# Optimization experiments

Hardware: AMD Instinct MI355X
Metric: run time of the kernel (lower is better)

## Reference

```python
import jax, jax.numpy as jnp
import numpy as np
from jax import lax

FILTER_SIZE = 3
C_IN = 128
C_OUT = 256
PAD = 1
STRIDE = 1


def setup_inputs() -> dict:
    key = jax.random.key(0)
    k1, k2 = jax.random.split(key)
    prev_a = jax.random.normal(k1, (32, 56, 56, C_IN), dtype=jnp.float32)
    # filter_w initialized ~ N(0, 1) as in the original tf.random.normal
    filter_w = jax.random.normal(k2, (FILTER_SIZE, FILTER_SIZE, C_IN, C_OUT), dtype=jnp.float32)
    filter_b = jnp.zeros((1, 1, 1, C_OUT), dtype=jnp.float32)
    return {"prev_a": prev_a, "filter_w": filter_w, "filter_b": filter_b}


def reference(prev_a, filter_w, filter_b):
    # NHWC input, HWIO filter -> NHWC output; same math as the nested-loop conv:
    # z[i,h,w,c] = sum(prev_a_pad[i, h*s:h*s+f, w*s:w*s+f, :] * W[:,:,:,c]) + b[c]
    z = lax.conv_general_dilated(
        prev_a,
        filter_w,
        window_strides=(STRIDE, STRIDE),
        padding=[(PAD, PAD), (PAD, PAD)],
        dimension_numbers=("NHWC", "HWIO", "NHWC"),
    )
    z = z + filter_b  # bias broadcast over (m, H, W)
    return jax.nn.relu(z)
```

## Files before the change

kernel.cpp:

```cpp
#include <hip/hip_runtime.h>
#include <hip/hip_bf16.h>


#define NIMG 32
#define HH 56
#define WW 56
#define PH 58
#define PW 58
#define CIN 128
#define COUT 256
#define KTOT 1152
#define PAD_ELEMS (NIMG * PH * PW * CIN)

#define BK 64
#define NT (KTOT / BK)
#define NBLK ((NIMG * HH * WW) / 256)

typedef __attribute__((ext_vector_type(8))) short bf16x8;
typedef __attribute__((ext_vector_type(4))) short s16x4;
typedef __attribute__((ext_vector_type(4))) float f32x4;

__device__ __forceinline__ short f2bf(float x) {
    union { __hip_bfloat16 b; short s; } u;
    u.b = __float2bfloat16(x);
    return u.s;
}

typedef const void __attribute__((address_space(1)))* gas1_t;
typedef void __attribute__((address_space(3)))* las3_t;
__device__ __forceinline__ void async16(short* lds_p, const short* g) {
    __builtin_amdgcn_global_load_lds((gas1_t)g, (las3_t)lds_p, 16, 0, 0);
}

__global__ __launch_bounds__(256) void pack_input(const float* __restrict__ in,
                                                  short* __restrict__ pad) {
    const int tid  = blockIdx.x * 256 + threadIdx.x;
    const int flat = tid * 8;
    const int c8   = flat & (CIN - 1);
    const int rest = flat >> 7;
    const int iw   = rest % PW;
    const int r2   = rest / PW;
    const int ih   = r2 % PH;
    const int img  = r2 / PH;
    bf16x8 v = (bf16x8)0;
    if (ih >= 1 && ih <= HH && iw >= 1 && iw <= WW) {
        const float* p = in + (((size_t)(img * HH + ih - 1) * WW + (iw - 1)) * CIN + c8);
        const float4 x0 = *(const float4*)p;
        const float4 x1 = *(const float4*)(p + 4);
        v.s0 = f2bf(x0.x); v.s1 = f2bf(x0.y); v.s2 = f2bf(x0.z); v.s3 = f2bf(x0.w);
        v.s4 = f2bf(x1.x); v.s5 = f2bf(x1.y); v.s6 = f2bf(x1.z); v.s7 = f2bf(x1.w);
    }
    *(bf16x8*)(pad + flat) = v;
}

__global__ __launch_bounds__(256) void pack_wgt(const float* __restrict__ w,
                                                short* __restrict__ wt) {
    __shared__ short tile[32][33];
    const int k0 = blockIdx.x * 32;
    const int n0 = blockIdx.y * 32;
    const int t  = threadIdx.x;
    {
        const int kl  = t >> 3;
        const int nl4 = (t & 7) * 4;
        const float4 x = *(const float4*)(w + (size_t)(k0 + kl) * COUT + n0 + nl4);
        tile[kl][nl4 + 0] = f2bf(x.x);
        tile[kl][nl4 + 1] = f2bf(x.y);
        tile[kl][nl4 + 2] = f2bf(x.z);
        tile[kl][nl4 + 3] = f2bf(x.w);
    }
    __syncthreads();
    {
        const int nl  = t >> 3;
        const int kl4 = (t & 7) * 4;
        s16x4 v;
        v.x = tile[kl4 + 0][nl];
        v.y = tile[kl4 + 1][nl];
        v.z = tile[kl4 + 2][nl];
        v.w = tile[kl4 + 3][nl];
        *(s16x4*)(wt + (size_t)(n0 + nl) * KTOT + k0 + kl4) = v;
    }
}

#define FENCE() asm volatile("" ::: "memory")
#define BARRIER() do { FENCE(); __builtin_amdgcn_s_barrier(); FENCE(); } while (0)
#define VMWAIT(N) asm volatile("s_waitcnt vmcnt(" #N ")" ::: "memory")
#define NOSTMT ((void)0)

__global__ __launch_bounds__(512, 2) void conv_mfma(const short* __restrict__ apad,
                                                    const short* __restrict__ bwt,
                                                    const float* __restrict__ bias,
                                                    float* __restrict__ out) {
    __shared__ short lds[65536];

    const int t  = threadIdx.x;
    const int l  = t & 63;
    const int w  = t >> 6;
    const int wm = w >> 2;
    const int wn = w & 3;
    const int fr = l & 15;
    const int fq = l >> 4;

    const int laneoff = fr * 32 + ((fq ^ ((fr >> 1) & 3))) * 8;
    const int kcs   = (t & 3) ^ ((t >> 3) & 3);
    const int wbase = w * 512;

    const int bid = blockIdx.x;
    const int swz = (bid & 7) * (NBLK / 8) + (bid >> 3);
    const int m0  = swz * 256;

    const int r0 = t >> 2;
    int abase0, abase1;
    {
        int m = m0 + r0;
        int img = m / (HH * WW), rem = m - img * (HH * WW);
        int oh = rem / WW, ow = rem - oh * WW;
        abase0 = ((img * PH + oh) * PW + ow) * CIN;
        m = m0 + r0 + 128;
        img = m / (HH * WW); rem = m - img * (HH * WW);
        oh = rem / WW; ow = rem - oh * WW;
        abase1 = ((img * PH + oh) * PW + ow) * CIN;
    }
    const int bbase0 = r0 * KTOT;
    const int bbase1 = (r0 + 128) * KTOT;

    f32x4 acc[8][4];
#pragma unroll
    for (int i = 0; i < 8; ++i)
#pragma unroll
        for (int j = 0; j < 4; ++j) { f32x4 z = {0.f, 0.f, 0.f, 0.f}; acc[i][j] = z; }

    bf16x8 af[8];

#define STAGE_A(KT, KH) do {                                                  \
        const int _tap = (KT) >> 1;                                           \
        const int _fh  = (_tap * 11) >> 5;                   \
        const int _fw  = _tap - 3 * _fh;                                      \
        const int _off = (_fh * PW + _fw) * CIN + ((KT) & 1) * 64             \
                         + (KH) * 32 + kcs * 8;                               \
        short* _l = lds + (((KT) & 1) * 2 + (KH)) * 8192 + wbase;             \
        async16(_l,        apad + abase0 + _off);                             \
        async16(_l + 4096, apad + abase1 + _off);                             \
    } while (0)

#define STAGE_B(KT, KH) do {                                                  \
        const int _off = (KT) * 64 + (KH) * 32 + kcs * 8;                     \
        short* _l = lds + 32768 + (((KT) & 1) * 2 + (KH)) * 8192 + wbase;     \
        async16(_l,        bwt + bbase0 + _off);                              \
        async16(_l + 4096, bwt + bbase1 + _off);                              \
    } while (0)

#define PHASE(BUF, KH, NH, STAGE_STMT, WAIT_STMT) do {                        \
        const short* _a = lds + ((BUF) * 2 + (KH)) * 8192;                    \
        const short* _b = lds + 32768 + ((BUF) * 2 + (KH)) * 8192;            \
        bf16x8 _bf0, _bf1;                                                    \
        if ((NH) == 0) {                                                      \
            _Pragma("unroll")                                                 \
            for (int _i = 0; _i < 8; ++_i)                                    \
                af[_i] = *(const bf16x8*)(_a + wm * 4096 + _i * 512 + laneoff); \
        }                                                                     \
        _bf0 = *(const bf16x8*)(_b + wn * 2048 + (NH) * 1024 +   0 + laneoff); \
        _bf1 = *(const bf16x8*)(_b + wn * 2048 + (NH) * 1024 + 512 + laneoff); \
        STAGE_STMT;                                                           \
        BARRIER();                                                            \
        __builtin_amdgcn_s_setprio(1);                                        \
        _Pragma("unroll")                                                     \
        for (int _i = 0; _i < 8; ++_i) {                                      \
            acc[_i][(NH)*2+0] = __builtin_amdgcn_mfma_f32_16x16x32_bf16(      \
                af[_i], _bf0, acc[_i][(NH)*2+0], 0, 0, 0);                    \
            acc[_i][(NH)*2+1] = __builtin_amdgcn_mfma_f32_16x16x32_bf16(      \
                af[_i], _bf1, acc[_i][(NH)*2+1], 0, 0, 0);                    \
        }                                                                     \
        __builtin_amdgcn_s_setprio(0);                                        \
        WAIT_STMT;                                                            \
        BARRIER();                                                            \
    } while (0)

    STAGE_A(0, 0); STAGE_B(0, 0);
    STAGE_A(0, 1); STAGE_B(0, 1);
    STAGE_A(1, 0); STAGE_B(1, 0);
    VMWAIT(8);
    BARRIER();

#pragma unroll 1
    for (int kt = 0; kt < NT - 2; kt += 2) {
        PHASE(0, 0, 0, STAGE_A(kt + 1, 1), NOSTMT);
        PHASE(0, 0, 1, STAGE_B(kt + 1, 1), VMWAIT(8));
        PHASE(0, 1, 0, STAGE_A(kt + 2, 0), NOSTMT);
        PHASE(0, 1, 1, STAGE_B(kt + 2, 0), VMWAIT(8));
        PHASE(1, 0, 0, STAGE_A(kt + 2, 1), NOSTMT);
        PHASE(1, 0, 1, STAGE_B(kt + 2, 1), VMWAIT(8));
        PHASE(1, 1, 0, STAGE_A(kt + 3, 0), NOSTMT);
        PHASE(1, 1, 1, STAGE_B(kt + 3, 0), VMWAIT(8));
    }
    PHASE(0, 0, 0, STAGE_A(NT - 1, 1), NOSTMT);
    PHASE(0, 0, 1, STAGE_B(NT - 1, 1), VMWAIT(8));
    PHASE(0, 1, 0, NOSTMT,             NOSTMT);
    PHASE(0, 1, 1, NOSTMT,             VMWAIT(4));
    PHASE(1, 0, 0, NOSTMT,             NOSTMT);
    PHASE(1, 0, 1, NOSTMT,             VMWAIT(0));
    PHASE(1, 1, 0, NOSTMT,             NOSTMT);
    PHASE(1, 1, 1, NOSTMT,             NOSTMT);

#pragma unroll
    for (int j = 0; j < 4; ++j) {
        const int n  = wn * 64 + j * 16 + fr;
        const float bj = bias[n];
#pragma unroll
        for (int i = 0; i < 8; ++i) {
            const int mr = m0 + wm * 128 + i * 16 + fq * 4;
#pragma unroll
            for (int r = 0; r < 4; ++r) {
                const float v = acc[i][j][r] + bj;
                out[(size_t)(mr + r) * COUT + n] = v > 0.f ? v : 0.f;
            }
        }
    }
#undef STAGE_A
#undef STAGE_B
#undef PHASE
}

extern "C" void kernel_launch(void* const* d_in, const int* in_sizes, int n_in,
                              void* d_out, int out_size, void* d_ws, size_t ws_size,
                              hipStream_t stream) {
    const float* in   = (const float*)d_in[0];
    const float* wgt  = (const float*)d_in[1];
    const float* bias = (const float*)d_in[2];
    float* out = (float*)d_out;

    short* pad = (short*)d_ws;
    short* wt  = (short*)d_ws + PAD_ELEMS;

    pack_input<<<PAD_ELEMS / 8 / 256, 256, 0, stream>>>(in, pad);
    pack_wgt<<<dim3(KTOT / 32, COUT / 32), 256, 0, stream>>>(wgt, wt);

    conv_mfma<<<NBLK, 512, 0, stream>>>(pad, wt, bias, out);
}
```

Before: 205.0 us.

## Shrink conv M-tile to 224 rows and restructure MFMA phases

Changes the block M-tile from 256 to 224 output pixels, so there are 448 blocks instead of 392 and each block does less work. The 2-blocks-per-CU slots on the device are used more evenly and the critical path per block gets shorter. The LDS layout, A staging and accumulator tiling are reworked to 7x4 fragments per wave. Each k-step now splits into one phase with 4 A rows and 4 B columns and a second phase with the remaining 3 A rows. Waves 6 and 7 issue redundant duplicate A loads into already-written slots. The lower ratio of MFMA work to loads per block may reduce efficiency.

```diff
diff --git a/kernel.cpp b/kernel.cpp
--- a/kernel.cpp
+++ b/kernel.cpp
@@ -12,9 +12,14 @@
 #define KTOT 1152
 #define PAD_ELEMS (NIMG * PH * PW * CIN)
 
+#define BM 224
 #define BK 64
 #define NT (KTOT / BK)
-#define NBLK ((NIMG * HH * WW) / 256)
+#define NBLK ((NIMG * HH * WW) / BM)
+
+#define AREG_SZ 7168
+#define BREG_BASE 28672
+#define BREG_SZ 8192
 
 typedef __attribute__((ext_vector_type(8))) short bf16x8;
 typedef __attribute__((ext_vector_type(4))) short s16x4;
@@ -90,7 +95,7 @@
                                                     const short* __restrict__ bwt,
                                                     const float* __restrict__ bias,
                                                     float* __restrict__ out) {
-    __shared__ short lds[65536];
+    __shared__ short lds[61440];
 
     const int t  = threadIdx.x;
     const int l  = t & 63;
@@ -101,12 +106,13 @@
     const int fq = l >> 4;
 
     const int laneoff = fr * 32 + ((fq ^ ((fr >> 1) & 3))) * 8;
-    const int kcs   = (t & 3) ^ ((t >> 3) & 3);
-    const int wbase = w * 512;
+    const int afb = wm * 3584;
+    const int bfb = wn * 2048;
+    const int kcs = (t & 3) ^ ((t >> 3) & 3);
 
     const int bid = blockIdx.x;
     const int swz = (bid & 7) * (NBLK / 8) + (bid >> 3);
-    const int m0  = swz * 256;
+    const int m0  = swz * BM;
 
     const int r0 = t >> 2;
     int abase0, abase1;
@@ -115,21 +121,26 @@
         int img = m / (HH * WW), rem = m - img * (HH * WW);
         int oh = rem / WW, ow = rem - oh * WW;
         abase0 = ((img * PH + oh) * PW + ow) * CIN;
-        m = m0 + r0 + 128;
-        img = m / (HH * WW); rem = m - img * (HH * WW);
-        oh = rem / WW; ow = rem - oh * WW;
-        abase1 = ((img * PH + oh) * PW + ow) * CIN;
-    }
+        if (t < 384) {
+            m = m0 + r0 + 128;
+            img = m / (HH * WW); rem = m - img * (HH * WW);
+            oh = rem / WW; ow = rem - oh * WW;
+            abase1 = ((img * PH + oh) * PW + ow) * CIN;
+        } else {
+            abase1 = abase0;
+        }
+    }
+    const int a2lds = (w < 6) ? (4096 + w * 512) : (w * 512);
     const int bbase0 = r0 * KTOT;
     const int bbase1 = (r0 + 128) * KTOT;
 
-    f32x4 acc[8][4];
-#pragma unroll
-    for (int i = 0; i < 8; ++i)
+    f32x4 acc[7][4];
+#pragma unroll
+    for (int i = 0; i < 7; ++i)
 #pragma unroll
         for (int j = 0; j < 4; ++j) { f32x4 z = {0.f, 0.f, 0.f, 0.f}; acc[i][j] = z; }
 
-    bf16x8 af[8];
+    bf16x8 af0[4], af1[3], bf[4];
 
 #define STAGE_A(KT, KH) do {                                                  \
         const int _tap = (KT) >> 1;                                           \
@@ -137,39 +148,55 @@
         const int _fw  = _tap - 3 * _fh;                                      \
         const int _off = (_fh * PW + _fw) * CIN + ((KT) & 1) * 64             \
                          + (KH) * 32 + kcs * 8;                               \
-        short* _l = lds + (((KT) & 1) * 2 + (KH)) * 8192 + wbase;             \
-        async16(_l,        apad + abase0 + _off);                             \
-        async16(_l + 4096, apad + abase1 + _off);                             \
+        short* _l = lds + ((((KT) & 1) << 1) + (KH)) * AREG_SZ;               \
+        async16(_l + w * 512, apad + abase0 + _off);                          \
+        async16(_l + a2lds,   apad + abase1 + _off);                          \
     } while (0)
 
 #define STAGE_B(KT, KH) do {                                                  \
         const int _off = (KT) * 64 + (KH) * 32 + kcs * 8;                     \
-        short* _l = lds + 32768 + (((KT) & 1) * 2 + (KH)) * 8192 + wbase;     \
-        async16(_l,        bwt + bbase0 + _off);                              \
-        async16(_l + 4096, bwt + bbase1 + _off);                              \
-    } while (0)
-
-#define PHASE(BUF, KH, NH, STAGE_STMT, WAIT_STMT) do {                        \
-        const short* _a = lds + ((BUF) * 2 + (KH)) * 8192;                    \
-        const short* _b = lds + 32768 + ((BUF) * 2 + (KH)) * 8192;            \
-        bf16x8 _bf0, _bf1;                                                    \
-        if ((NH) == 0) {                                                      \
+        short* _l = lds + BREG_BASE + ((((KT) & 1) << 1) + (KH)) * BREG_SZ;   \
+        async16(_l + w * 512,        bwt + bbase0 + _off);                    \
+        async16(_l + 4096 + w * 512, bwt + bbase1 + _off);                    \
+    } while (0)
+
+#define PH_MH0(BUF, KH, STAGE_STMT, WAIT_STMT) do {                           \
+        const short* _a = lds + (((BUF) << 1) + (KH)) * AREG_SZ;              \
+        const short* _b = lds + BREG_BASE + (((BUF) << 1) + (KH)) * BREG_SZ;  \
+        _Pragma("unroll")                                                     \
+        for (int _i = 0; _i < 4; ++_i)                                        \
+            af0[_i] = *(const bf16x8*)(_a + afb + _i * 512 + laneoff);        \
+        _Pragma("unroll")                                                     \
+        for (int _j = 0; _j < 4; ++_j)                                        \
+            bf[_j] = *(const bf16x8*)(_b + bfb + _j * 512 + laneoff);         \
+        STAGE_STMT;                                                           \
+        BARRIER();                                                            \
+        __builtin_amdgcn_s_setprio(1);                                        \
+        _Pragma("unroll")                                                     \
+        for (int _i = 0; _i < 4; ++_i)                                        \
             _Pragma("unroll")                                                 \
-            for (int _i = 0; _i < 8; ++_i)                                    \
-                af[_i] = *(const bf16x8*)(_a + wm * 4096 + _i * 512 + laneoff); \
-        }                                                                     \
-        _bf0 = *(const bf16x8*)(_b + wn * 2048 + (NH) * 1024 +   0 + laneoff); \
-        _bf1 = *(const bf16x8*)(_b + wn * 2048 + (NH) * 1024 + 512 + laneoff); \
+            for (int _j = 0; _j < 4; ++_j)                                    \
+                acc[_i][_j] = __builtin_amdgcn_mfma_f32_16x16x32_bf16(        \
+                    af0[_i], bf[_j], acc[_i][_j], 0, 0, 0);                   \
+        __builtin_amdgcn_s_setprio(0);                                        \
+        WAIT_STMT;                                                            \
+        BARRIER();                                                            \
+    } while (0)
+
+#define PH_MH1(BUF, KH, STAGE_STMT, WAIT_STMT) do {                           \
+        const short* _a = lds + (((BUF) << 1) + (KH)) * AREG_SZ;              \
+        _Pragma("unroll")                                                     \
+        for (int _i = 0; _i < 3; ++_i)                                        \
+            af1[_i] = *(const bf16x8*)(_a + afb + 2048 + _i * 512 + laneoff); \
         STAGE_STMT;                                                           \
         BARRIER();                                                            \
         __builtin_amdgcn_s_setprio(1);                                        \
         _Pragma("unroll")                                                     \
-        for (int _i = 0; _i < 8; ++_i) {                                      \
-            acc[_i][(NH)*2+0] = __builtin_amdgcn_mfma_f32_16x16x32_bf16(      \
-                af[_i], _bf0, acc[_i][(NH)*2+0], 0, 0, 0);                    \
-            acc[_i][(NH)*2+1] = __builtin_amdgcn_mfma_f32_16x16x32_bf16(      \
-                af[_i], _bf1, acc[_i][(NH)*2+1], 0, 0, 0);                    \
-        }                                                                     \
+        for (int _i = 0; _i < 3; ++_i)                                        \
+            _Pragma("unroll")                                                 \
+            for (int _j = 0; _j < 4; ++_j)                                    \
+                acc[4 + _i][_j] = __builtin_amdgcn_mfma_f32_16x16x32_bf16(    \
+                    af1[_i], bf[_j], acc[4 + _i][_j], 0, 0, 0);               \
         __builtin_amdgcn_s_setprio(0);                                        \
         WAIT_STMT;                                                            \
         BARRIER();                                                            \
@@ -183,31 +210,31 @@
 
 #pragma unroll 1
     for (int kt = 0; kt < NT - 2; kt += 2) {
-        PHASE(0, 0, 0, STAGE_A(kt + 1, 1), NOSTMT);
-        PHASE(0, 0, 1, STAGE_B(kt + 1, 1), VMWAIT(8));
-        PHASE(0, 1, 0, STAGE_A(kt + 2, 0), NOSTMT);
-        PHASE(0, 1, 1, STAGE_B(kt + 2, 0), VMWAIT(8));
-        PHASE(1, 0, 0, STAGE_A(kt + 2, 1), NOSTMT);
-        PHASE(1, 0, 1, STAGE_B(kt + 2, 1), VMWAIT(8));
-        PHASE(1, 1, 0, STAGE_A(kt + 3, 0), NOSTMT);
-        PHASE(1, 1, 1, STAGE_B(kt + 3, 0), VMWAIT(8));
-    }
-    PHASE(0, 0, 0, STAGE_A(NT - 1, 1), NOSTMT);
-    PHASE(0, 0, 1, STAGE_B(NT - 1, 1), VMWAIT(8));
-    PHASE(0, 1, 0, NOSTMT,             NOSTMT);
-    PHASE(0, 1, 1, NOSTMT,             VMWAIT(4));
-    PHASE(1, 0, 0, NOSTMT,             NOSTMT);
-    PHASE(1, 0, 1, NOSTMT,             VMWAIT(0));
-    PHASE(1, 1, 0, NOSTMT,             NOSTMT);
-    PHASE(1, 1, 1, NOSTMT,             NOSTMT);
+        PH_MH0(0, 0, STAGE_A(kt + 1, 1), NOSTMT);
+        PH_MH1(0, 0, STAGE_B(kt + 1, 1), VMWAIT(8));
+        PH_MH0(0, 1, STAGE_A(kt + 2, 0), NOSTMT);
+        PH_MH1(0, 1, STAGE_B(kt + 2, 0), VMWAIT(8));
+        PH_MH0(1, 0, STAGE_A(kt + 2, 1), NOSTMT);
+        PH_MH1(1, 0, STAGE_B(kt + 2, 1), VMWAIT(8));
+        PH_MH0(1, 1, STAGE_A(kt + 3, 0), NOSTMT);
+        PH_MH1(1, 1, STAGE_B(kt + 3, 0), VMWAIT(8));
+    }
+    PH_MH0(0, 0, STAGE_A(NT - 1, 1), NOSTMT);
+    PH_MH1(0, 0, STAGE_B(NT - 1, 1), VMWAIT(8));
+    PH_MH0(0, 1, NOSTMT,             NOSTMT);
+    PH_MH1(0, 1, NOSTMT,             VMWAIT(4));
+    PH_MH0(1, 0, NOSTMT,             NOSTMT);
+    PH_MH1(1, 0, NOSTMT,             VMWAIT(0));
+    PH_MH0(1, 1, NOSTMT,             NOSTMT);
+    PH_MH1(1, 1, NOSTMT,             NOSTMT);
 
 #pragma unroll
     for (int j = 0; j < 4; ++j) {
         const int n  = wn * 64 + j * 16 + fr;
         const float bj = bias[n];
 #pragma unroll
-        for (int i = 0; i < 8; ++i) {
-            const int mr = m0 + wm * 128 + i * 16 + fq * 4;
+        for (int i = 0; i < 7; ++i) {
+            const int mr = m0 + wm * 112 + i * 16 + fq * 4;
 #pragma unroll
             for (int r = 0; r < 4; ++r) {
                 const float v = acc[i][j][r] + bj;
@@ -217,7 +244,8 @@
     }
 #undef STAGE_A
 #undef STAGE_B
-#undef PHASE
+#undef PH_MH0
+#undef PH_MH1
 }
 
 extern "C" void kernel_launch(void* const* d_in, const int* in_sizes, int n_in,
```

Result: faster. 199.1 us (-2.9%).
